# Performance work log

Measured on AMD Instinct MI355X. Metric: run time of the kernel, lower is better.

The kernel has to match this reference:

```python
import math
import jax, jax.numpy as jnp
import numpy as np
from jax.scipy.special import erf

BATCH, SEQ, DIM = 2, 4096, 128
EMA_HEADS, DQK, DV = 16, 64, 256
NUM_BUCKETS, MAX_DIST = 32, 128


def _next_fast_len(n):
    # smallest 5-smooth integer >= n (matches scipy.fftpack.next_fast_len)
    while True:
        m = n
        for p in (2, 3, 5):
            while m % p == 0:
                m //= p
        if m == 1:
            return n
        n += 1


def _laplacian_attn(x):
    mu = math.sqrt(0.5)
    std = math.sqrt(0.25 * math.pi)
    return 0.5 * (1.0 + erf((x - mu) / (std * math.sqrt(2.0))))


def _rel_pos_bias(table, n, scale):
    # causal T5 relative position bias, bucket(q_pos - k_pos)
    pos = jnp.arange(n)
    rel = jnp.maximum(pos[:, None] - pos[None, :], 0)  # [n, n], >= 0
    max_exact = NUM_BUCKETS // 2
    is_small = rel < max_exact
    val_large = max_exact + (
        jnp.log(jnp.maximum(rel, 1).astype(jnp.float32) / max_exact)
        / math.log(MAX_DIST / max_exact) * (NUM_BUCKETS - max_exact)
    ).astype(jnp.int32)
    val_large = jnp.minimum(val_large, NUM_BUCKETS - 1)
    bucket = jnp.where(is_small, rel, val_large)
    return table[bucket, 0] * scale  # [n, n]


def _conv1d_fft(x, K, n):
    # x: [b, n, h, d] (fft over axis 1), K: [n, h] (fft over axis 0)
    fast_len = _next_fast_len(2 * n - 1)
    f_x = jnp.fft.rfft(x, n=fast_len, axis=1)
    f_K = jnp.fft.rfft(K, n=fast_len, axis=0)
    out = jnp.fft.irfft(f_x * jnp.conj(f_K)[None, :, :, None], fast_len, axis=1)
    out = jnp.roll(out, -1, axis=1)
    return out[:, fast_len - n:]  # [b, n, h, d]


def _forward(x, expansion, reduction, alphas, dampen, Wqk, bqk, gamma, beta,
             Wv, bv, rel_table, Wr, br, Wu, bu, Wh, Uh, bh):
    b, n, d = x.shape
    # ---- multi-headed EMA (causal -> unidirectional) via FFT conv ----
    xe = jnp.einsum('bnd,hd->bnhd', x, expansion)
    a = jax.nn.sigmoid(alphas)            # [h]
    dm = jax.nn.sigmoid(dampen)           # [h]
    powers = jnp.arange(n - 1, -1, -1, dtype=x.dtype)  # reversed powers
    K = a * ((1.0 - a) * dm) ** powers[:, None]        # [n, h]
    conv = _conv1d_fft(xe, K, n)
    ema = jnp.einsum('bnhd,hd->bnd', conv, reduction)  # [b, n, d]
    # ---- single-headed attention (chunk_size=-1 -> one chunk), v from x ----
    qk = jax.nn.silu(ema @ Wqk + bqk)     # [b, n, dqk]
    q = qk * gamma[0] + beta[0]
    k = qk * gamma[1] + beta[1]
    v = jax.nn.silu(x @ Wv + bv)          # [b, n, dv]
    scale = 1.0 / n                       # laplacian_attn_fn scaling
    sim = jnp.einsum('bid,bjd->bij', q, k) * scale
    sim = sim + _rel_pos_bias(rel_table, n, DQK ** 0.5)
    attn = _laplacian_attn(sim)
    causal_mask = jnp.triu(jnp.ones((n, n), dtype=bool), 1)
    attn = jnp.where(causal_mask, 0.0, attn)  # laplacian: zero after activation
    attn_out = jnp.einsum('bij,bjd->bid', attn, v)  # [b, n, dv]
    # ---- gating + output ----
    reset_gate = jax.nn.silu(ema @ Wr + br)         # [b, n, dv]
    update_gate = jax.nn.sigmoid(ema @ Wu + bu)     # [b, n, d]
    gated = attn_out * reset_gate
    H = jax.nn.silu(ema @ Wh + gated @ Uh + bh)     # [b, n, d]
    return update_gate * H + (1.0 - update_gate) * x


def setup_inputs() -> dict:
    key = jax.random.key(0)
    ks = jax.random.split(key, 18)
    def rn(i, shape, s=1.0):
        return jax.random.normal(ks[i], shape, dtype=jnp.float32) * s
    return dict(
        x=rn(0, (BATCH, SEQ, DIM)),
        expansion=rn(1, (EMA_HEADS, DIM), 0.2),
        reduction=rn(2, (EMA_HEADS, DIM), 0.2),
        alphas=rn(3, (EMA_HEADS,)),
        dampen=rn(4, (EMA_HEADS,)),
        Wqk=rn(5, (DIM, DQK), 0.05), bqk=rn(6, (DQK,), 0.02),
        gamma=rn(7, (2, DQK), 0.02), beta=jnp.zeros((2, DQK), jnp.float32),
        Wv=rn(8, (DIM, DV), 0.05), bv=rn(9, (DV,), 0.02),
        rel_table=rn(10, (NUM_BUCKETS, 1), 0.02),
        Wr=rn(11, (DIM, DV), 0.05), br=rn(12, (DV,), 0.02),
        Wu=rn(13, (DIM, DIM), 0.05), bu=rn(14, (DIM,), 0.02),
        Wh=rn(15, (DIM, DIM), 0.05), Uh=rn(16, (DV, DIM), 0.05),
        bh=rn(17, (DIM,), 0.02),
    )


def reference(x, expansion, reduction, alphas, dampen, Wqk, bqk, gamma, beta,
              Wv, bv, rel_table, Wr, br, Wu, bu, Wh, Uh, bh):
    return _forward(x, expansion, reduction, alphas, dampen, Wqk, bqk, gamma,
                    beta, Wv, bv, rel_table, Wr, br, Wu, bu, Wh, Uh, bh)
```

## Files before the change

### kernel.cpp

```cpp
#include <hip/hip_runtime.h>
#include <cstdint>
#include <cmath>

#define B_ 2
#define N_ 4096
#define D_ 128
#define H_ 16
#define DQK_ 64
#define DV_ 256

typedef float    f4_t  __attribute__((ext_vector_type(4)));
typedef float    f16f  __attribute__((ext_vector_type(16)));
typedef _Float16 h4_t  __attribute__((ext_vector_type(4)));
typedef _Float16 h8_t  __attribute__((ext_vector_type(8)));

__device__ __forceinline__ float sigmoidf_(float z) { return 1.f/(1.f + expf(-z)); }
__device__ __forceinline__ float siluf_(float z)    { return z/(1.f + expf(-z)); }
__device__ __forceinline__ f16f zero16() {
  f16f z;
#pragma unroll
  for (int i = 0; i < 16; ++i) z[i] = 0.f;
  return z;
}

__global__ void ema_phase1(const float* __restrict__ x, const float* __restrict__ expansion,
                           const float* __restrict__ alphas, const float* __restrict__ dampen,
                           float* __restrict__ F, _Float16* __restrict__ xh) {
  int bid = blockIdx.x;
  int dg = bid & 7, c = (bid >> 3) & 63, b = bid >> 9;
  int h = threadIdx.x & 15, dl = threadIdx.x >> 4;
  int d = dg*16 + dl;
  float a  = sigmoidf_(alphas[h]);
  float dm = sigmoidf_(dampen[h]);
  float q  = (1.f - a)*dm;
  float coef = a * expansion[h*D_ + d];
  __shared__ float xs[64][16];
  {
    int e = threadIdx.x;
    int t = e >> 2, seg = e & 3;
    const float* xp = x + ((size_t)b*N_ + c*64 + t)*D_ + dg*16 + seg*4;
    f4_t v = *(const f4_t*)xp;
    *(f4_t*)&xs[t][seg*4] = v;
    h4_t hv;
#pragma unroll
    for (int j = 0; j < 4; ++j) hv[j] = (_Float16)v[j];
    *(h4_t*)(xh + ((size_t)b*N_ + c*64 + t)*D_ + dg*16 + seg*4) = hv;
  }
  __syncthreads();
  float s = 0.f;
#pragma unroll
  for (int t = 0; t < 64; ++t) s = fmaf(q, s, coef*xs[t][dl]);
  F[(((size_t)b*H_ + h)*D_ + d)*64 + c] = s;
}

__global__ void ema_carry(const float* __restrict__ F, const float* __restrict__ alphas,
                          const float* __restrict__ dampen, float* __restrict__ carry) {
  int idx = blockIdx.x*256 + threadIdx.x;
  int h = (idx >> 7) & 15;
  float a  = sigmoidf_(alphas[h]);
  float dm = sigmoidf_(dampen[h]);
  float q  = (1.f - a)*dm;
  float qL = q;
#pragma unroll
  for (int i = 0; i < 6; ++i) qL *= qL;
  const float* Fp = F + (size_t)idx*64;
  float* cp = carry + (size_t)idx*64;
  float s = 0.f;
  for (int cc = 0; cc < 64; ++cc) { cp[cc] = s; s = fmaf(qL, s, Fp[cc]); }
}

__global__ void ema_phase2(const float* __restrict__ x, const float* __restrict__ expansion,
                           const float* __restrict__ reduction,
                           const float* __restrict__ alphas, const float* __restrict__ dampen,
                           const float* __restrict__ carry, _Float16* __restrict__ emah) {
  int bid = blockIdx.x;
  int dg = bid & 7, c = (bid >> 3) & 63, b = bid >> 9;
  int h = threadIdx.x & 15, dl = threadIdx.x >> 4;
  int d = dg*16 + dl;
  float a  = sigmoidf_(alphas[h]);
  float dm = sigmoidf_(dampen[h]);
  float q  = (1.f - a)*dm;
  float coef = a * expansion[h*D_ + d];
  float red  = reduction[h*D_ + d];
  __shared__ float xs[64][16];
  {
    int e = threadIdx.x;
    int t = e >> 2, seg = e & 3;
    const float* xp = x + ((size_t)b*N_ + c*64 + t)*D_ + dg*16 + seg*4;
    *(f4_t*)&xs[t][seg*4] = *(const f4_t*)xp;
  }
  __syncthreads();
  float s = carry[(((size_t)b*H_ + h)*D_ + d)*64 + c];
  for (int t = 0; t < 64; ++t) {
    s = fmaf(q, s, coef*xs[t][dl]);
    float v = red * s;
    v += __shfl_xor(v, 1); v += __shfl_xor(v, 2);
    v += __shfl_xor(v, 4); v += __shfl_xor(v, 8);
    if (h == 0) emah[((size_t)b*N_ + c*64 + t)*D_ + d] = (_Float16)v;
  }
}

__global__ void prep_all(const float* __restrict__ Wqk, const float* __restrict__ Wv,
                         const float* __restrict__ Wr, const float* __restrict__ Wu,
                         const float* __restrict__ Wh,
                         const float* __restrict__ bqk, const float* __restrict__ bv,
                         const float* __restrict__ br, const float* __restrict__ bu,
                         const float* __restrict__ bh,
                         const float* __restrict__ Uh, const float* __restrict__ rel_table,
                         _Float16* __restrict__ Wt, float* __restrict__ bcat,
                         _Float16* __restrict__ Uht, float* __restrict__ bias2T) {
  int idx = blockIdx.x*256 + threadIdx.x;
  if (idx < 832*128) {
    int c = idx >> 7, d = idx & 127;
    const float* W; const float* bias; int ncol, cl;
    if (c < 64)       { W=Wqk; bias=bqk; ncol=64;  cl=c; }
    else if (c < 320) { W=Wv;  bias=bv;  ncol=256; cl=c-64; }
    else if (c < 576) { W=Wr;  bias=br;  ncol=256; cl=c-320; }
    else if (c < 704) { W=Wu;  bias=bu;  ncol=128; cl=c-576; }
    else              { W=Wh;  bias=bh;  ncol=128; cl=c-704; }
    Wt[idx] = (_Float16)W[d*ncol + cl];
    if (d == 0) bcat[c] = bias[cl];
  } else if (idx < 832*128 + 32768) {
    int i2 = idx - 832*128;
    int k = i2 >> 7, c = i2 & 127;
    Uht[(size_t)c*256 + k] = (_Float16)Uh[i2];
  } else if (idx < 832*128 + 32768 + 4096) {
    int r = idx - (832*128 + 32768);
    int bucket;
    if (r < 16) bucket = r;
    else {
      double v = log((double)r / 16.0) / log(8.0) * 16.0;
      bucket = 16 + (int)v;
      if (bucket > 31) bucket = 31;
    }
    bias2T[r] = (rel_table[bucket]*8.0f - 0.70710678f) * 1.1283792f;
  }
}

__global__ __launch_bounds__(256) void linear_mfma(
    const _Float16* __restrict__ emah, const _Float16* __restrict__ xh,
    const _Float16* __restrict__ Wt, const float* __restrict__ bcat,
    const float* __restrict__ gamma, const float* __restrict__ beta,
    _Float16* __restrict__ qh, _Float16* __restrict__ kh, _Float16* __restrict__ vTt,
    float* __restrict__ resetb, float* __restrict__ updateb, float* __restrict__ hemab) {
  int slab = blockIdx.x % 13, rt = blockIdx.x / 13;
  int tid = threadIdx.x;
  int lane = tid & 63, w = tid >> 6;
  int lr = lane & 15, lg = lane >> 4;
  int mode = (slab==0)?0:(slab<5)?1:(slab<9)?2:(slab<11)?3:4;
  const _Float16* src = (mode==1) ? xh : emah;
  __shared__ _Float16 As[64][136];
  __shared__ _Float16 Ws[64][136];
  {
    const h8_t* s8 = (const h8_t*)(src + (size_t)rt*64*D_);
#pragma unroll
    for (int i = 0; i < 4; ++i) {
      int idx = tid + i*256;
      int row = idx >> 4, seg = idx & 15;
      *(h8_t*)&As[row][seg*8] = s8[idx];
    }
    const h8_t* w8 = (const h8_t*)(Wt + (size_t)slab*64*D_);
#pragma unroll
    for (int i = 0; i < 4; ++i) {
      int idx = tid + i*256;
      int row = idx >> 4, seg = idx & 15;
      *(h8_t*)&Ws[row][seg*8] = w8[idx];
    }
  }
  __syncthreads();
  h4_t af[8];
#pragma unroll
  for (int ks = 0; ks < 8; ++ks) af[ks] = *(const h4_t*)&As[w*16 + lr][ks*16 + lg*4];
  int row0 = rt*64 + w*16 + lg*4;
#pragma unroll
  for (int ns = 0; ns < 4; ++ns) {
    f4_t acc = (f4_t){0.f,0.f,0.f,0.f};
#pragma unroll
    for (int ks = 0; ks < 8; ++ks) {
      h4_t bf = *(const h4_t*)&Ws[ns*16 + lr][ks*16 + lg*4];
      acc = __builtin_amdgcn_mfma_f32_16x16x16f16(af[ks], bf, acc, 0, 0, 0);
    }
    int c = slab*64 + ns*16 + lr;
    float bias = bcat[c];
    if (mode == 0) {
      float g0 = gamma[c], g1 = gamma[64+c], be0 = beta[c], be1 = beta[64+c];
#pragma unroll
      for (int r = 0; r < 4; ++r) {
        float qk = siluf_(acc[r] + bias);
        size_t row = row0 + r;
        qh[row*DQK_ + c] = (_Float16)(qk*g0 + be0);
        kh[row*DQK_ + c] = (_Float16)(qk*g1 + be1);
      }
    } else if (mode == 1) {
      int cl = c - 64;
      int bb = row0 >> 12, rl = row0 & 4095;
      h4_t vv;
#pragma unroll
      for (int r = 0; r < 4; ++r) vv[r] = (_Float16)siluf_(acc[r] + bias);
      *(h4_t*)&vTt[(((size_t)bb*128 + (rl>>5))*256 + cl)*32 + (rl&31)] = vv;
    } else if (mode == 2) {
      int cl = c - 320;
#pragma unroll
      for (int r = 0; r < 4; ++r) resetb[(size_t)(row0 + r)*DV_ + cl] = siluf_(acc[r] + bias);
    } else if (mode == 3) {
      int cl = c - 576;
#pragma unroll
      for (int r = 0; r < 4; ++r) updateb[(size_t)(row0 + r)*D_ + cl] = sigmoidf_(acc[r] + bias);
    } else {
      int cl = c - 704;
#pragma unroll
      for (int r = 0; r < 4; ++r) hemab[(size_t)(row0 + r)*D_ + cl] = acc[r] + bias;
    }
  }
}

__global__ __launch_bounds__(256, 3) void attn_kernel(
    const _Float16* __restrict__ qh, const _Float16* __restrict__ kh,
    const _Float16* __restrict__ vTt, const float* __restrict__ bias2T,
    _Float16* __restrict__ attnp) {
  int bid = blockIdx.x;
  int it = 63 - (bid >> 5);
  int rem = bid & 31;
  int s = rem >> 1, b = rem & 1;
  int a = it >> 2, r = it & 3;
  int nblk = a + 1;
  if (s >= nblk) return;
  int T = 2*it + 2;
  int tlo = (s*T)/nblk, thi = ((s+1)*T)/nblk;
  int nt = thi - tlo;
  int base = it + 2*a*(a-1) + r*a;
  int slot = base + s;
  int i0 = it * 64;
  int tid = threadIdx.x;
  int lane = tid & 63, w = tid >> 6;
  int ih = w & 1, dvh = w >> 1;
  int lm = lane & 31, lg = lane >> 5;

  __shared__ __align__(16) char lds[2][22784];
  __shared__ float biasW[320];

  int jmax = thi*32 - 1, jmin = tlo*32;
  int dlo = i0 - jmax;
  int cnt = 64 + jmax - jmin;
  for (int k = tid; k < cnt; k += 256) {
    int d = dlo + k;
    biasW[k] = d < 0 ? -1e38f : bias2T[d];
  }

  h4_t qf[8];
  {
    const _Float16* qp = qh + ((size_t)b*N_ + i0 + ih*32 + lm)*DQK_ + 4*lg;
#pragma unroll
    for (int ksq = 0; ksq < 8; ++ksq) qf[ksq] = *(const h4_t*)(qp + 8*ksq);
  }

  f16f accO[4];
#pragma unroll
  for (int i = 0; i < 4; ++i) accO[i] = zero16();

  const _Float16* kbase = kh + (size_t)b*N_*DQK_;
  const _Float16* vbase = vTt + (size_t)b*128*8192;
  int kj = tid >> 3, kseg = tid & 7;

  h8_t k8r, vreg[4];
#define ISSUE_(JT) { \
  k8r = *(const h8_t*)(kbase + (size_t)((JT)*32 + kj)*DQK_ + kseg*8); \
  const _Float16* vp_ = vbase + (size_t)(JT)*8192 + tid*32; \
  _Pragma("unroll") for (int i = 0; i < 4; ++i) vreg[i] = *(const h8_t*)(vp_ + i*8); }

#define COMMIT_(BUF) { \
  char* buf_ = (BUF); \
  char* ka_ = buf_ + kj*136 + kseg*16; \
  *(h4_t*)ka_ = __builtin_shufflevector(k8r, k8r, 0,1,2,3); \
  *(h4_t*)(ka_ + 8) = __builtin_shufflevector(k8r, k8r, 4,5,6,7); \
  char* va_ = buf_ + 4352 + tid*72; \
  _Pragma("unroll") for (int i = 0; i < 4; ++i) { \
    *(h4_t*)(va_ + i*16) = __builtin_shufflevector(vreg[i], vreg[i], 0,1,2,3); \
    *(h4_t*)(va_ + i*16 + 8) = __builtin_shufflevector(vreg[i], vreg[i], 4,5,6,7); } }

  ISSUE_(tlo); COMMIT_(lds[0]);
  if (nt > 1) ISSUE_(tlo + 1);
  __syncthreads();

  const float C1 = 1.1283792f / 4096.f;
  int ibase = i0 + ih*32 + lm;
#pragma unroll 1
  for (int t = 0; t < nt; ++t) {
    const char* kb = lds[t & 1];
    const char* vb = lds[t & 1] + 4352;
    __builtin_amdgcn_s_setprio(1);
    f16f accS = zero16();
#pragma unroll
    for (int ksq = 0; ksq < 8; ++ksq) {
      h4_t kf = *(const h4_t*)(kb + lm*136 + 16*ksq + 8*lg);
      accS = __builtin_amdgcn_mfma_f32_32x32x8f16(kf, qf[ksq], accS, 0, 0, 0);
    }
    __builtin_amdgcn_s_setprio(0);
    h4_t pa[4];
    {
      int idx0 = ibase - dlo - (tlo + t)*32 - 4*lg;
#pragma unroll
      for (int rr = 0; rr < 16; ++rr) {
        float tt = fmaf(accS[rr], C1, biasW[idx0 - 8*(rr>>2) - (rr&3)]);
        float e = tt*fmaf(tt*tt, -0.101797f, -2.304877f);
        float u = exp2f(e);
        float pv = __builtin_amdgcn_rcpf(1.f + u);
        pa[rr>>2][rr&3] = (_Float16)pv;
      }
    }
    __builtin_amdgcn_s_setprio(1);
#pragma unroll
    for (int ks = 0; ks < 4; ++ks) {
#pragma unroll
      for (int dvb = 0; dvb < 4; ++dvb) {
        h4_t vf = *(const h4_t*)(vb + (dvh*128 + dvb*32 + lm)*72 + 16*ks + 8*lg);
        accO[dvb] = __builtin_amdgcn_mfma_f32_32x32x8f16(pa[ks], vf, accO[dvb], 0, 0, 0);
      }
    }
    __builtin_amdgcn_s_setprio(0);
    if (t+1 < nt) COMMIT_(lds[(t+1) & 1]);
    if (t+2 < nt) ISSUE_(tlo + t + 2);
    __syncthreads();
  }
#undef ISSUE_
#undef COMMIT_

  _Float16* op = attnp + ((size_t)b*544 + slot)*(64*256);
#pragma unroll
  for (int dvb = 0; dvb < 4; ++dvb) {
    int col = dvh*128 + dvb*32 + lm;
#pragma unroll
    for (int rr = 0; rr < 16; ++rr) {
      int row = ih*32 + 8*(rr>>2) + 4*lg + (rr&3);
      op[(size_t)row*256 + col] = (_Float16)accO[dvb][rr];
    }
  }
}

__global__ void combine_gated(const _Float16* __restrict__ attnp, const float* __restrict__ resetb,
                              _Float16* __restrict__ gatedh) {
  size_t fi = (size_t)blockIdx.x*256 + threadIdx.x;
  int c4 = (int)(fi & 63);
  int rr = (int)(fi >> 6);
  int b = rr >> 12, n = rr & 4095;
  int it = n >> 6, rowLocal = n & 63;
  int a = it >> 2, r = it & 3;
  int nblk = a + 1;
  int base = it + 2*a*(a-1) + r*a;
  const _Float16* ap = attnp + ((size_t)b*544 + base)*16384 + rowLocal*256 + c4*4;
  f4_t acc = (f4_t){0.f,0.f,0.f,0.f};
  for (int s2 = 0; s2 < nblk; ++s2) {
    h4_t pv = *(const h4_t*)(ap + (size_t)s2*16384);
#pragma unroll
    for (int j = 0; j < 4; ++j) acc[j] += (float)pv[j];
  }
  f4_t rg = ((const f4_t*)resetb)[fi];
  f4_t g = acc * rg;
  h4_t hg;
#pragma unroll
  for (int j = 0; j < 4; ++j) hg[j] = (_Float16)g[j];
  *(h4_t*)(gatedh + fi*4) = hg;
}

__global__ __launch_bounds__(256) void final_mfma(
    const _Float16* __restrict__ gatedh, const _Float16* __restrict__ Uht,
    const float* __restrict__ hemab, const float* __restrict__ updateb,
    const float* __restrict__ x, float* __restrict__ out) {
  int rt = blockIdx.x >> 1, cs = blockIdx.x & 1;
  int tid = threadIdx.x;
  int lane = tid & 63, w = tid >> 6;
  int lr = lane & 15, lg = lane >> 4;
  int row0 = rt*64, c0 = cs*64;
  __shared__ _Float16 As[64][136];
  __shared__ _Float16 Ws[64][136];
  f4_t acc[4];
#pragma unroll
  for (int ns = 0; ns < 4; ++ns) acc[ns] = (f4_t){0.f,0.f,0.f,0.f};
#pragma unroll
  for (int kc = 0; kc < 2; ++kc) {
    __syncthreads();
#pragma unroll
    for (int i = 0; i < 4; ++i) {
      int idx = tid + i*256;
      int row = idx >> 4, seg = idx & 15;
      *(h8_t*)&As[row][seg*8] =
          *(const h8_t*)(gatedh + (size_t)(row0 + row)*DV_ + kc*128 + seg*8);
      *(h8_t*)&Ws[row][seg*8] =
          *(const h8_t*)(Uht + (size_t)(c0 + row)*DV_ + kc*128 + seg*8);
    }
    __syncthreads();
    h4_t af[8];
#pragma unroll
    for (int ks = 0; ks < 8; ++ks) af[ks] = *(const h4_t*)&As[w*16 + lr][ks*16 + lg*4];
#pragma unroll
    for (int ns = 0; ns < 4; ++ns) {
#pragma unroll
      for (int ks = 0; ks < 8; ++ks) {
        h4_t bf = *(const h4_t*)&Ws[ns*16 + lr][ks*16 + lg*4];
        acc[ns] = __builtin_amdgcn_mfma_f32_16x16x16f16(af[ks], bf, acc[ns], 0, 0, 0);
      }
    }
  }
  int orow = row0 + w*16 + lg*4;
#pragma unroll
  for (int ns = 0; ns < 4; ++ns) {
    int col = c0 + ns*16 + lr;
#pragma unroll
    for (int r = 0; r < 4; ++r) {
      size_t o = (size_t)(orow + r)*D_ + col;
      float z = acc[ns][r] + hemab[o];
      float Hv = siluf_(z);
      float u  = updateb[o];
      out[o] = u*Hv + (1.f - u)*x[o];
    }
  }
}

extern "C" void kernel_launch(void* const* d_in, const int* in_sizes, int n_in,
                              void* d_out, int out_size, void* d_ws, size_t ws_size,
                              hipStream_t stream) {
  (void)in_sizes; (void)n_in; (void)out_size; (void)ws_size;
  const float* x         = (const float*)d_in[0];
  const float* expansion = (const float*)d_in[1];
  const float* reduction = (const float*)d_in[2];
  const float* alphas    = (const float*)d_in[3];
  const float* dampen    = (const float*)d_in[4];
  const float* Wqk       = (const float*)d_in[5];
  const float* bqk       = (const float*)d_in[6];
  const float* gamma     = (const float*)d_in[7];
  const float* beta      = (const float*)d_in[8];
  const float* Wv        = (const float*)d_in[9];
  const float* bv        = (const float*)d_in[10];
  const float* rel_table = (const float*)d_in[11];
  const float* Wr        = (const float*)d_in[12];
  const float* br        = (const float*)d_in[13];
  const float* Wu        = (const float*)d_in[14];
  const float* bu        = (const float*)d_in[15];
  const float* Wh        = (const float*)d_in[16];
  const float* Uh        = (const float*)d_in[17];
  const float* bh        = (const float*)d_in[18];
  float* out = (float*)d_out;

  char* p = (char*)d_ws;
  size_t off = 0;
  auto alloc = [&](size_t bytes) -> char* {
    char* r = p + off;
    off += (bytes + 255) & ~(size_t)255;
    return r;
  };
  float*    F      = (float*)alloc((size_t)B_*H_*D_*64*4);
  float*    carry  = (float*)alloc((size_t)B_*H_*D_*64*4);
  _Float16* emah   = (_Float16*)alloc((size_t)B_*N_*D_*2);
  _Float16* xh     = (_Float16*)alloc((size_t)B_*N_*D_*2);
  float*    bias2T = (float*)alloc((size_t)N_*4);
  _Float16* Wt     = (_Float16*)alloc((size_t)832*128*2);
  float*    bcat   = (float*)alloc((size_t)832*4);
  _Float16* Uht    = (_Float16*)alloc((size_t)D_*DV_*2);
  _Float16* qh     = (_Float16*)alloc((size_t)B_*N_*DQK_*2);
  _Float16* kh     = (_Float16*)alloc((size_t)B_*N_*DQK_*2);
  _Float16* vTt    = (_Float16*)alloc((size_t)B_*DV_*N_*2);
  float*    resetb = (float*)alloc((size_t)B_*N_*DV_*4);
  float*    updateb= (float*)alloc((size_t)B_*N_*D_*4);
  float*    hemab  = (float*)alloc((size_t)B_*N_*D_*4);
  _Float16* gatedh = (_Float16*)alloc((size_t)B_*N_*DV_*2);
  _Float16* attnp  = (_Float16*)alloc((size_t)B_*544*64*256*2);

  prep_all<<<560, 256, 0, stream>>>(Wqk, Wv, Wr, Wu, Wh, bqk, bv, br, bu, bh,
                                    Uh, rel_table, Wt, bcat, Uht, bias2T);
  ema_phase1<<<1024, 256, 0, stream>>>(x, expansion, alphas, dampen, F, xh);
  ema_carry<<<16, 256, 0, stream>>>(F, alphas, dampen, carry);
  ema_phase2<<<1024, 256, 0, stream>>>(x, expansion, reduction, alphas, dampen, carry, emah);
  linear_mfma<<<128*13, 256, 0, stream>>>(emah, xh, Wt, bcat, gamma, beta,
                                          qh, kh, vTt, resetb, updateb, hemab);
  attn_kernel<<<2048, 256, 0, stream>>>(qh, kh, vTt, bias2T, attnp);
  combine_gated<<<2048, 256, 0, stream>>>(attnp, resetb, gatedh);
  final_mfma<<<256, 256, 0, stream>>>(gatedh, Uht, hemab, updateb, x, out);
}
```

Baseline: 120.3 us.

## Specialize waves into score producers and loaders, sharing probabilities via LDS

Splits the four waves in the attention kernel by role. The two waves with dvh==0 compute the QK scores and the probability transform once and publish them to LDS. The other two waves take over all global-to-LDS staging of K and V and then read the shared probabilities back. This removes the duplicate score MFMAs and transcendental work that both dvh halves used to do, and overlaps global loads with compute. In exchange it adds a second barrier per tile, an extra LDS round trip for P, and more registers per loader thread, which could unbalance the waves.

```diff
diff --git a/kernel.cpp b/kernel.cpp
--- a/kernel.cpp
+++ b/kernel.cpp
@@ -233,22 +233,26 @@
   int i0 = it * 64;
   int tid = threadIdx.x;
   int lane = tid & 63, w = tid >> 6;
-  int ih = w & 1, dvh = w >> 1;
+  int ih = w & 1;
+  int dvh = w >> 1;
+  bool prod = (dvh == 0);
   int lm = lane & 31, lg = lane >> 5;
 
-  __shared__ __align__(16) char lds[2][22784];
+  __shared__ __align__(16) char Vb[2][18432];
+  __shared__ __align__(16) char Kb[2][4352];
+  __shared__ __align__(16) char Pb[2][2560];
   __shared__ float biasW[320];
 
-  int jmax = thi*32 - 1, jmin = tlo*32;
-  int dlo = i0 - jmax;
-  int cnt = 64 + jmax - jmin;
+  int jmaxv = thi*32 - 1;
+  int dlo = i0 - jmaxv;
+  int cnt = 64 + jmaxv - tlo*32;
   for (int k = tid; k < cnt; k += 256) {
     int d = dlo + k;
     biasW[k] = d < 0 ? -1e38f : bias2T[d];
   }
 
   h4_t qf[8];
-  {
+  if (prod) {
     const _Float16* qp = qh + ((size_t)b*N_ + i0 + ih*32 + lm)*DQK_ + 4*lg;
 #pragma unroll
     for (int ksq = 0; ksq < 8; ++ksq) qf[ksq] = *(const h4_t*)(qp + 8*ksq);
@@ -260,44 +264,54 @@
 
   const _Float16* kbase = kh + (size_t)b*N_*DQK_;
   const _Float16* vbase = vTt + (size_t)b*128*8192;
-  int kj = tid >> 3, kseg = tid & 7;
-
-  h8_t k8r, vreg[4];
+  int st = tid & 127;
+  int kr = st >> 2, ks16 = st & 3;
+
+  h8_t k8a, k8b, vr[8];
 #define ISSUE_(JT) { \
-  k8r = *(const h8_t*)(kbase + (size_t)((JT)*32 + kj)*DQK_ + kseg*8); \
-  const _Float16* vp_ = vbase + (size_t)(JT)*8192 + tid*32; \
-  _Pragma("unroll") for (int i = 0; i < 4; ++i) vreg[i] = *(const h8_t*)(vp_ + i*8); }
-
-#define COMMIT_(BUF) { \
-  char* buf_ = (BUF); \
-  char* ka_ = buf_ + kj*136 + kseg*16; \
-  *(h4_t*)ka_ = __builtin_shufflevector(k8r, k8r, 0,1,2,3); \
-  *(h4_t*)(ka_ + 8) = __builtin_shufflevector(k8r, k8r, 4,5,6,7); \
-  char* va_ = buf_ + 4352 + tid*72; \
+  const _Float16* kp_ = kbase + (size_t)((JT)*32 + kr)*DQK_ + ks16*16; \
+  k8a = *(const h8_t*)kp_; k8b = *(const h8_t*)(kp_ + 8); \
+  const _Float16* vp_ = vbase + (size_t)(JT)*8192 + st*32; \
+  _Pragma("unroll") for (int i = 0; i < 4; ++i) vr[i] = *(const h8_t*)(vp_ + i*8); \
+  _Pragma("unroll") for (int i = 0; i < 4; ++i) vr[4+i] = *(const h8_t*)(vp_ + 4096 + i*8); }
+
+#define COMMIT_(BI) { \
+  char* kb_ = Kb[BI] + kr*136 + ks16*32; \
+  *(h4_t*)kb_        = __builtin_shufflevector(k8a, k8a, 0,1,2,3); \
+  *(h4_t*)(kb_ + 8)  = __builtin_shufflevector(k8a, k8a, 4,5,6,7); \
+  *(h4_t*)(kb_ + 16) = __builtin_shufflevector(k8b, k8b, 0,1,2,3); \
+  *(h4_t*)(kb_ + 24) = __builtin_shufflevector(k8b, k8b, 4,5,6,7); \
+  char* va_ = Vb[BI] + st*72; \
   _Pragma("unroll") for (int i = 0; i < 4; ++i) { \
-    *(h4_t*)(va_ + i*16) = __builtin_shufflevector(vreg[i], vreg[i], 0,1,2,3); \
-    *(h4_t*)(va_ + i*16 + 8) = __builtin_shufflevector(vreg[i], vreg[i], 4,5,6,7); } }
-
-  ISSUE_(tlo); COMMIT_(lds[0]);
-  if (nt > 1) ISSUE_(tlo + 1);
+    *(h4_t*)(va_ + i*16)     = __builtin_shufflevector(vr[i], vr[i], 0,1,2,3); \
+    *(h4_t*)(va_ + i*16 + 8) = __builtin_shufflevector(vr[i], vr[i], 4,5,6,7); } \
+  char* vb2_ = Vb[BI] + (st + 128)*72; \
+  _Pragma("unroll") for (int i = 0; i < 4; ++i) { \
+    *(h4_t*)(vb2_ + i*16)     = __builtin_shufflevector(vr[4+i], vr[4+i], 0,1,2,3); \
+    *(h4_t*)(vb2_ + i*16 + 8) = __builtin_shufflevector(vr[4+i], vr[4+i], 4,5,6,7); } }
+
+  if (!prod) {
+    ISSUE_(tlo);
+    COMMIT_(0);
+    if (nt > 1) ISSUE_(tlo + 1);
+  }
   __syncthreads();
 
   const float C1 = 1.1283792f / 4096.f;
   int ibase = i0 + ih*32 + lm;
 #pragma unroll 1
   for (int t = 0; t < nt; ++t) {
-    const char* kb = lds[t & 1];
-    const char* vb = lds[t & 1] + 4352;
-    __builtin_amdgcn_s_setprio(1);
-    f16f accS = zero16();
-#pragma unroll
-    for (int ksq = 0; ksq < 8; ++ksq) {
-      h4_t kf = *(const h4_t*)(kb + lm*136 + 16*ksq + 8*lg);
-      accS = __builtin_amdgcn_mfma_f32_32x32x8f16(kf, qf[ksq], accS, 0, 0, 0);
-    }
-    __builtin_amdgcn_s_setprio(0);
     h4_t pa[4];
-    {
+    if (prod) {
+      const char* kb = Kb[t & 1];
+      __builtin_amdgcn_s_setprio(1);
+      f16f accS = zero16();
+#pragma unroll
+      for (int ksq = 0; ksq < 8; ++ksq) {
+        h4_t kf = *(const h4_t*)(kb + lm*136 + 16*ksq + 8*lg);
+        accS = __builtin_amdgcn_mfma_f32_32x32x8f16(kf, qf[ksq], accS, 0, 0, 0);
+      }
+      __builtin_amdgcn_s_setprio(0);
       int idx0 = ibase - dlo - (tlo + t)*32 - 4*lg;
 #pragma unroll
       for (int rr = 0; rr < 16; ++rr) {
@@ -307,7 +321,20 @@
         float pv = __builtin_amdgcn_rcpf(1.f + u);
         pa[rr>>2][rr&3] = (_Float16)pv;
       }
-    }
+      char* pp = Pb[ih] + lane*40;
+#pragma unroll
+      for (int k2 = 0; k2 < 4; ++k2) *(h4_t*)(pp + k2*8) = pa[k2];
+    } else {
+      if (t+1 < nt) COMMIT_((t+1) & 1);
+      if (t+2 < nt) ISSUE_(tlo + t + 2);
+    }
+    __syncthreads();
+    if (!prod) {
+      const char* pp = Pb[ih] + lane*40;
+#pragma unroll
+      for (int k2 = 0; k2 < 4; ++k2) pa[k2] = *(const h4_t*)(pp + k2*8);
+    }
+    const char* vb = Vb[t & 1];
     __builtin_amdgcn_s_setprio(1);
 #pragma unroll
     for (int ks = 0; ks < 4; ++ks) {
@@ -318,8 +345,6 @@
       }
     }
     __builtin_amdgcn_s_setprio(0);
-    if (t+1 < nt) COMMIT_(lds[(t+1) & 1]);
-    if (t+2 < nt) ISSUE_(tlo + t + 2);
     __syncthreads();
   }
 #undef ISSUE_
```

Measured after the change: 113.8 us. -5.4%, faster.
